# Optimization experiments

Hardware: AMD Instinct MI355X
Metric: run time of the kernel (lower is better)

The kernel has to match this reference:

```python
import jax, jax.numpy as jnp
import numpy as np

N = 50000; FIN = 64; H = 128; E = 800000; T = 8
P = 250000; D = 500000; G = 20000; V = 2000; O = 2


def _mp(h, Ws, Wn, b, edge_src, edge_dst, n):
    # mean-aggregation message passing: relu(h Ws + mean_neigh(h) Wn + b)
    deg = jax.ops.segment_sum(jnp.ones(edge_dst.shape[0], h.dtype), edge_dst, n)
    agg = jax.ops.segment_sum(h[edge_src], edge_dst, n) / jnp.maximum(deg, 1.0)[:, None]
    return jax.nn.relu(h @ Ws + agg @ Wn + b)


def _forward(x, W_enc_self, W_enc_nei, b_enc, W2_self, W2_nei, b2, Wd1, bd1, Wd2, bd2,
             counts, edge_src, edge_dst, place_idx, src_idx, t_idx, dst_nodes, dst_seg,
             group_id, variant_of_group):
    n = x.shape[0]
    p = place_idx.shape[0]
    g = variant_of_group.shape[0]
    v = counts.shape[0]
    # first encoder, then T sequential second_encoder applications (feature generations)
    h0 = _mp(x, W_enc_self, W_enc_nei, b_enc, edge_src, edge_dst, n)

    def step(h, _):
        h2 = _mp(h, W2_self, W2_nei, b2, edge_src, edge_dst, n)
        return h2, h2

    _, hs = jax.lax.scan(step, h0, None, length=T)
    feats = jnp.concatenate([h0[None], hs], axis=0)  # [T+1, N, H]

    # gather (place, src) features at the generation index of each prediction
    place_f = feats[t_idx, place_idx]                 # [P, H]
    src_f = feats[t_idx, src_idx]                     # [P, H]
    # dst feature = sum over the destination set of each prediction
    dst_f = jax.ops.segment_sum(feats[t_idx[dst_seg], dst_nodes], dst_seg, p)  # [P, H]

    cat = jnp.concatenate([place_f, src_f, dst_f], axis=-1)  # [P, 3H]
    logits = jax.nn.relu(cat @ Wd1 + bd1) @ Wd2 + bd2        # [P, O]
    logprob = jax.nn.log_softmax(logits, axis=-1)            # [P, O]

    # prev_prob: inclusive running sum of per-step logprob sums within each variant
    group_sums = jax.ops.segment_sum(logprob, group_id, g)   # [G, O]
    cum = jnp.cumsum(group_sums, axis=0)
    var_tot = jax.ops.segment_sum(group_sums, variant_of_group, v)
    var_excl = jnp.cumsum(var_tot, axis=0) - var_tot
    within = cum - var_excl[variant_of_group]                # [G, O]
    prev = within[group_id]                                  # [P, O]

    logc = jnp.log(counts / jnp.sum(counts))                 # log(count/total) per variant
    add = logprob + prev + logc[variant_of_group[group_id]][:, None]
    return jnp.zeros((n, logits.shape[-1]), x.dtype).at[place_idx].add(add)


def setup_inputs() -> dict:
    ks = jax.random.split(jax.random.key(0), 24)
    s = jnp.float32(0.05)
    f32 = jnp.float32
    i32 = jnp.int32
    return {
        "x": jax.random.normal(ks[0], (N, FIN), f32),
        "W_enc_self": jax.random.normal(ks[1], (FIN, H), f32) * s,
        "W_enc_nei": jax.random.normal(ks[2], (FIN, H), f32) * s,
        "b_enc": jax.random.normal(ks[3], (H,), f32) * s,
        "W2_self": jax.random.normal(ks[4], (H, H), f32) * s,
        "W2_nei": jax.random.normal(ks[5], (H, H), f32) * s,
        "b2": jax.random.normal(ks[6], (H,), f32) * s,
        "Wd1": jax.random.normal(ks[7], (3 * H, 3 * H), f32) * s,
        "bd1": jax.random.normal(ks[8], (3 * H,), f32) * s,
        "Wd2": jax.random.normal(ks[9], (3 * H, O), f32) * s,
        "bd2": jax.random.normal(ks[10], (O,), f32) * s,
        "counts": jax.random.uniform(ks[11], (V,), f32) + 0.5,
        "edge_src": jax.random.randint(ks[12], (E,), 0, N, i32),
        "edge_dst": jax.random.randint(ks[13], (E,), 0, N, i32),
        "place_idx": jax.random.randint(ks[14], (P,), 0, N, i32),
        "src_idx": jax.random.randint(ks[15], (P,), 0, N, i32),
        "t_idx": jax.random.randint(ks[16], (P,), 0, T + 1, i32),
        "dst_nodes": jax.random.randint(ks[17], (D,), 0, N, i32),
        "dst_seg": jnp.sort(jax.random.randint(ks[18], (D,), 0, P, i32)),
        "group_id": jnp.sort(jax.random.randint(ks[19], (P,), 0, G, i32)),
        "variant_of_group": jnp.sort(jax.random.randint(ks[20], (G,), 0, V, i32)),
    }


def reference(x, W_enc_self, W_enc_nei, b_enc, W2_self, W2_nei, b2, Wd1, bd1, Wd2, bd2,
              counts, edge_src, edge_dst, place_idx, src_idx, t_idx, dst_nodes, dst_seg,
              group_id, variant_of_group):
    return _forward(x, W_enc_self, W_enc_nei, b_enc, W2_self, W2_nei, b2, Wd1, bd1, Wd2, bd2,
                    counts, edge_src, edge_dst, place_idx, src_idx, t_idx, dst_nodes, dst_seg,
                    group_id, variant_of_group)
```

## Files before the change

kernel.cpp:

```cpp
#include <hip/hip_runtime.h>
#include <math.h>

#define NN 50000
#define FINN 64
#define HD 128
#define EE 800000
#define TT 8
#define PP 250000
#define DD 500000
#define GG 20000
#define VV 2000
#define OO 2

#define DEC_GRID 256
#define DEC_TILES ((PP + 63) / 64)

typedef short short8 __attribute__((ext_vector_type(8)));
typedef float f32x4 __attribute__((ext_vector_type(4)));

__device__ __forceinline__ unsigned short f2bf(float f) {
    unsigned int u = __float_as_uint(f);
    u += 0x7fffu + ((u >> 16) & 1u);
    return (unsigned short)(u >> 16);
}
__device__ __forceinline__ float bf2f(unsigned short u) {
    return __uint_as_float(((unsigned int)u) << 16);
}

__device__ __forceinline__ unsigned char q8(float f) {
    unsigned short u = f2bf(f);
    unsigned int e = (u >> 7) & 0xffu;
    unsigned int s = (u >> 8) & 0x80u;
    if (e < 121u) return (unsigned char)s;
    unsigned int m = u & 0x7fu;
    unsigned int m3 = m >> 4, rr = m & 0xfu;
    m3 += (rr > 8u) || (rr == 8u && (m3 & 1u));
    unsigned int ee = e - 120u;
    if (m3 == 8u) { m3 = 0u; ++ee; }
    if (ee > 15u || (ee == 15u && m3 == 7u)) { ee = 15u; m3 = 6u; }
    return (unsigned char)(s | (ee << 3) | m3);
}
__device__ __forceinline__ unsigned int dq1(unsigned int b) {
    unsigned int t = b & 0x7fu;
    unsigned int r = ((b & 0x80u) << 8) | ((t << 4) + 0x3C00u);
    return t ? r : 0u;
}

struct us8 { unsigned short v[8]; };

__device__ __forceinline__ void gload_lds16(const void* g, void* l) {
    __builtin_amdgcn_global_load_lds((__attribute__((address_space(1))) void*)g,
                                     (__attribute__((address_space(3))) void*)l, 16, 0, 0);
}

__global__ void count_k(const int* __restrict__ idx, int* __restrict__ counts, int n) {
    int i = blockIdx.x * blockDim.x + threadIdx.x;
    if (i < n) atomicAdd(&counts[idx[i]], 1);
}

__global__ void blk_sum_k(const int* __restrict__ counts, int n, int* __restrict__ bsum) {
    __shared__ int buf[256];
    int t = threadIdx.x, i = blockIdx.x * 256 + t;
    buf[t] = (i < n) ? counts[i] : 0;
    __syncthreads();
    for (int off = 128; off > 0; off >>= 1) {
        if (t < off) buf[t] += buf[t + off];
        __syncthreads();
    }
    if (t == 0) bsum[blockIdx.x] = buf[0];
}

__global__ void scan_small_k(const int* __restrict__ bsum, int nb, int* __restrict__ boff) {
    __shared__ int buf[256];
    int t = threadIdx.x;
    int v = (t < nb) ? bsum[t] : 0;
    buf[t] = v;
    __syncthreads();
    for (int off = 1; off < 256; off <<= 1) {
        int u = (t >= off) ? buf[t - off] : 0;
        __syncthreads();
        buf[t] += u;
        __syncthreads();
    }
    if (t < nb) boff[t] = buf[t] - v;
}

__global__ void rowptr_fill_k(const int* __restrict__ counts, const int* __restrict__ boff,
                              int n, int* __restrict__ rowptr, int total) {
    __shared__ int buf[256];
    int t = threadIdx.x, i = blockIdx.x * 256 + t;
    int v = (i < n) ? counts[i] : 0;
    buf[t] = v;
    __syncthreads();
    for (int off = 1; off < 256; off <<= 1) {
        int u = (t >= off) ? buf[t - off] : 0;
        __syncthreads();
        buf[t] += u;
        __syncthreads();
    }
    if (i < n) rowptr[i] = boff[blockIdx.x] + buf[t] - v;
    if (i == 0) rowptr[n] = total;
}

__global__ void lb_rowptr_k(const int* __restrict__ arr, int n, int* __restrict__ rowptr, int m) {
    int i = blockIdx.x * blockDim.x + threadIdx.x;
    if (i > m) return;
    int lo = 0, hi = n;
    while (lo < hi) {
        int mid = (lo + hi) >> 1;
        if (arr[mid] < i) lo = mid + 1; else hi = mid;
    }
    rowptr[i] = lo;
}

__global__ void fill_csr_k(const int* __restrict__ esrc, const int* __restrict__ edst,
                           const int* __restrict__ rowptr, int* __restrict__ cursor,
                           int* __restrict__ outi, int n) {
    int e = blockIdx.x * blockDim.x + threadIdx.x;
    if (e < n) {
        int d = edst[e];
        int pos = atomicAdd(&cursor[d], 1);
        outi[rowptr[d] + pos] = esrc[e];
    }
}

__global__ void hist9_k(const int* __restrict__ t_idx, int* __restrict__ hist) {
    __shared__ int l[9];
    if (threadIdx.x < 9) l[threadIdx.x] = 0;
    __syncthreads();
    int p = blockIdx.x * 256 + threadIdx.x;
    if (p < PP) atomicAdd(&l[t_idx[p]], 1);
    __syncthreads();
    if (threadIdx.x < 9) atomicAdd(&hist[threadIdx.x], l[threadIdx.x]);
}

__global__ void scan9_k(const int* __restrict__ hist, int* __restrict__ boff9) {
    if (threadIdx.x == 0) {
        int a = 0;
        for (int i = 0; i < 9; ++i) { boff9[i] = a; a += hist[i]; }
        boff9[9] = a;
    }
}

__global__ void bucket_perm_k(const int* __restrict__ t_idx, const int* __restrict__ boff9,
                              int* __restrict__ cursor9, int* __restrict__ pperm) {
    __shared__ int lcnt[9];
    __shared__ int lbase[9];
    int tid = threadIdx.x;
    int p = blockIdx.x * 256 + tid;
    if (tid < 9) lcnt[tid] = 0;
    __syncthreads();
    int t = 0, lr = 0;
    bool ok = p < PP;
    if (ok) {
        t = t_idx[p];
        lr = atomicAdd(&lcnt[t], 1);
    }
    __syncthreads();
    if (tid < 9) lbase[tid] = atomicAdd(&cursor9[tid], lcnt[tid]);
    __syncthreads();
    if (ok) pperm[boff9[t] + lbase[t] + lr] = p;
}

__global__ void prep_k(const float* __restrict__ x,
                       const float* __restrict__ Wes, const float* __restrict__ Wen,
                       const float* __restrict__ W2s, const float* __restrict__ W2n,
                       const float* __restrict__ Wd1,
                       unsigned short* __restrict__ xb, unsigned short* __restrict__ wenc_t,
                       unsigned short* __restrict__ w2_t, unsigned short* __restrict__ wd1t,
                       unsigned char* __restrict__ wd1tq) {
    int i = blockIdx.x * 256 + threadIdx.x;
    if (i < NN * FINN) xb[i] = f2bf(x[i]);
    if (i < HD * 2 * FINN) {
        int c = i / (2 * FINN), k = i - c * (2 * FINN);
        wenc_t[i] = f2bf((k < FINN) ? Wes[k * HD + c] : Wen[(k - FINN) * HD + c]);
    }
    if (i < HD * 2 * HD) {
        int c = i / (2 * HD), k = i - c * (2 * HD);
        w2_t[i] = f2bf((k < HD) ? W2s[k * HD + c] : W2n[(k - HD) * HD + c]);
    }
    if (i < 384 * 384) {
        int n = i / 384, k = i - n * 384;
        float v = Wd1[k * 384 + n];
        wd1t[i] = f2bf(v);
        wd1tq[i] = q8(v);
    }
}

template <int KIN>
__launch_bounds__(256)
__global__ void mpf_k(const unsigned short* __restrict__ hin,
                      const int* __restrict__ rowptr, const int* __restrict__ csr_src,
                      const unsigned short* __restrict__ Wt, const float* __restrict__ bias,
                      unsigned short* __restrict__ hout, unsigned char* __restrict__ houtq) {
    constexpr int CPL = KIN / 64;
    __shared__ unsigned short sm[32 * KIN];
    int tid = threadIdx.x;
    int r = tid >> 3;
    int sl = tid & 7;
    int node = blockIdx.x * 32 + r;
    int rx = r & 7;

    if (node < NN) {
        int s = rowptr[node], e = rowptr[node + 1];
        float acc[8 * CPL] = {};
        int i = s, iB = s + 1;
        int srcA = (i < e) ? csr_src[i] : 0;
        int srcB = (iB < e) ? csr_src[iB] : 0;
        while (i < e) {
            bool hB = iB < e;
            us8 vA0, vA1, vB0, vB1;
            vA0 = *(const us8*)&hin[(size_t)srcA * KIN + sl * (8 * CPL)];
            if constexpr (CPL == 2) vA1 = *(const us8*)&hin[(size_t)srcA * KIN + sl * 16 + 8];
            if (hB) {
                vB0 = *(const us8*)&hin[(size_t)srcB * KIN + sl * (8 * CPL)];
                if constexpr (CPL == 2) vB1 = *(const us8*)&hin[(size_t)srcB * KIN + sl * 16 + 8];
            }
            int iN = i + 2, iN2 = i + 3;
            srcA = (iN < e) ? csr_src[iN] : 0;
            srcB = (iN2 < e) ? csr_src[iN2] : 0;
#pragma unroll
            for (int j = 0; j < 8; ++j) acc[j] += bf2f(vA0.v[j]);
            if constexpr (CPL == 2)
#pragma unroll
                for (int j = 0; j < 8; ++j) acc[8 + j] += bf2f(vA1.v[j]);
            if (hB) {
#pragma unroll
                for (int j = 0; j < 8; ++j) acc[j] += bf2f(vB0.v[j]);
                if constexpr (CPL == 2)
#pragma unroll
                    for (int j = 0; j < 8; ++j) acc[8 + j] += bf2f(vB1.v[j]);
            }
            i = iN; iB = iN2;
        }
        float d = fmaxf((float)(e - s), 1.f);
        us8 o0, o1;
#pragma unroll
        for (int j = 0; j < 8; ++j) o0.v[j] = f2bf(acc[j] / d);
        int c0 = sl * CPL;
        *(us8*)&sm[r * KIN + ((c0 ^ rx) * 8)] = o0;
        if constexpr (CPL == 2) {
#pragma unroll
            for (int j = 0; j < 8; ++j) o1.v[j] = f2bf(acc[8 + j] / d);
            *(us8*)&sm[r * KIN + (((c0 + 1) ^ rx) * 8)] = o1;
        }
    }
    __syncthreads();

    int lane = tid & 63, w = tid >> 6;
    int cc = lane & 15, gq = lane >> 4;
    constexpr int K = 2 * KIN;
    int rloc = (w & 1) * 16 + cc;
    int rowA = blockIdx.x * 32 + rloc;
    bool rowok = rowA < NN;
    const unsigned short* hrow = hin + (size_t)rowA * KIN;
    int ch = (w >> 1) * 64;
    int rlx = rloc & 7;

    f32x4 acc2[4];
#pragma unroll
    for (int t = 0; t < 4; ++t) acc2[t] = (f32x4){0.f, 0.f, 0.f, 0.f};

#pragma unroll
    for (int k0 = 0; k0 < K; k0 += 32) {
        int k = k0 + gq * 8;
        short8 a = {0, 0, 0, 0, 0, 0, 0, 0};
        if (rowok) {
            if (k0 < KIN) a = *(const short8*)(hrow + k);
            else {
                int chunk = (k - KIN) >> 3;
                a = *(const short8*)&sm[rloc * KIN + ((chunk ^ rlx) * 8)];
            }
        }
#pragma unroll
        for (int t = 0; t < 4; ++t) {
            short8 b = *(const short8*)&Wt[(size_t)(ch + t * 16 + cc) * K + k];
            acc2[t] = __builtin_amdgcn_mfma_f32_16x16x32_bf16(a, b, acc2[t], 0, 0, 0);
        }
    }
#pragma unroll
    for (int t = 0; t < 4; ++t) {
        int col = ch + t * 16 + cc;
        float b1 = bias[col];
#pragma unroll
        for (int rj = 0; rj < 4; ++rj) {
            int grow = blockIdx.x * 32 + (w & 1) * 16 + gq * 4 + rj;
            if (grow < NN) {
                float v = fmaxf(acc2[t][rj] + b1, 0.f);
                hout[(size_t)grow * HD + col] = f2bf(v);
                houtq[(size_t)grow * HD + col] = q8(v);
            }
        }
    }
}

__launch_bounds__(256)
__global__ void dst_sum2q_k(const unsigned char* __restrict__ featsq,
                            const int* __restrict__ t_idx, const int* __restrict__ dst_nodes,
                            const int* __restrict__ dst_rowptr, const int* __restrict__ pperm,
                            unsigned char* __restrict__ dstcq) {
    int tid = threadIdx.x;
    int grp = tid >> 4;
    int fl = tid & 15;
    int pi = blockIdx.x * 16 + grp;
    if (pi >= PP) return;
    int p = pperm[pi];
    long t = t_idx[p];
    const unsigned char* base = featsq + (size_t)t * NN * HD;
    int s = dst_rowptr[p], e = dst_rowptr[p + 1];
    float acc[8] = {};
    int i = s;
    int n0 = (i < e) ? dst_nodes[i] : 0;
    int n1 = (i + 1 < e) ? dst_nodes[i + 1] : 0;
    while (i < e) {
        bool h1 = (i + 1) < e;
        unsigned long long v0 = *(const unsigned long long*)&base[(size_t)n0 * HD + fl * 8];
        unsigned long long v1 = 0;
        if (h1) v1 = *(const unsigned long long*)&base[(size_t)n1 * HD + fl * 8];
        int i2 = i + 2, i3 = i + 3;
        n0 = (i2 < e) ? dst_nodes[i2] : 0;
        n1 = (i3 < e) ? dst_nodes[i3] : 0;
#pragma unroll
        for (int j = 0; j < 8; ++j)
            acc[j] += bf2f((unsigned short)dq1((unsigned int)(v0 >> (8 * j)) & 0xffu));
        if (h1) {
#pragma unroll
            for (int j = 0; j < 8; ++j)
                acc[j] += bf2f((unsigned short)dq1((unsigned int)(v1 >> (8 * j)) & 0xffu));
        }
        i = i2;
    }
    unsigned long long ov = 0;
#pragma unroll
    for (int j = 0; j < 8; ++j) ov |= (unsigned long long)q8(acc[j]) << (8 * j);
    *(unsigned long long*)&dstcq[(size_t)pi * HD + fl * 8] = ov;
}

__global__ void
__attribute__((amdgpu_flat_work_group_size(512, 512), amdgpu_waves_per_eu(2, 2)))
dec10_k(const unsigned char* __restrict__ featsq,
        const unsigned char* __restrict__ dstcq,
        const int* __restrict__ place_idx, const int* __restrict__ src_idx,
        const int* __restrict__ t_idx, const int* __restrict__ group_id,
        const int* __restrict__ pperm,
        const unsigned char* __restrict__ wd1tq,
        const float* __restrict__ bd1, const float* __restrict__ Wd2,
        const float* __restrict__ bd2, float* __restrict__ logprob,
        float* __restrict__ group_sums) {
    __shared__ unsigned char buf[3][192 * 128];
    __shared__ unsigned int rb[3][192];
    __shared__ float lpart[3][8][64][2];

    int tid = threadIdx.x;
    int lane = tid & 63, w = tid >> 6;
    int cc = lane & 15, gq = lane >> 4;
    int bid = blockIdx.x;

    int row = min(tid, 191);
    int sec = row >> 6, pl = row & 63;
    const int* nptr = (sec == 0) ? place_idx : src_idx;
    unsigned int dstc_off = (unsigned int)(dstcq - featsq);

    int nt = (DEC_TILES - 1 - bid) / DEC_GRID + 1;
    float b20 = bd2[0], b21 = bd2[1];

    if (tid < 192) {
#pragma unroll
        for (int s3 = 0; s3 < 3; ++s3) {
            int pic = min((bid + s3 * DEC_GRID) * 64 + pl, PP - 1);
            int p = pperm[pic];
            rb[s3][tid] = (sec == 2) ? (dstc_off + (unsigned int)pic * 128u)
                                     : (unsigned int)(((unsigned)t_idx[p] * NN + (unsigned)nptr[p]) * 128u);
        }
    }
    int p3 = pperm[min((bid + 3 * DEC_GRID) * 64 + pl, PP - 1)];
    int tOld = t_idx[p3], nOld = nptr[p3];
    int pCur = pperm[min((bid + 4 * DEC_GRID) * 64 + pl, PP - 1)];
    int opPP = 0, opP = 0, ogP = 0;

    unsigned long long breg[36];
    float b1r[3], w0r[3], w1r[3];
    {
        const unsigned char* bbase = wd1tq + ((long)(w * 48 + cc) * 384 + gq * 8);
#pragma unroll
        for (int kk = 0; kk < 12; ++kk)
#pragma unroll
            for (int t = 0; t < 3; ++t)
                breg[kk * 3 + t] = *(const unsigned long long*)(bbase + (long)t * 16 * 384 + kk * 32);
#pragma unroll
        for (int t = 0; t < 3; ++t) {
            int col = w * 48 + t * 16 + cc;
            b1r[t] = bd1[col];
            w0r[t] = Wd2[col * 2 + 0];
            w1r[t] = Wd2[col * 2 + 1];
        }
    }
    __syncthreads();

    int rsub8 = lane >> 3, chunk8 = lane & 7;

#define STAGE(slot_)                                                                 \
    {                                                                                \
        _Pragma("unroll")                                                            \
        for (int i = 0; i < 3; ++i) {                                                \
            int r = w * 24 + i * 8 + rsub8;                                          \
            const unsigned char* src = featsq + rb[slot_][r] +                       \
                                       ((unsigned)(chunk8 ^ (r & 7)) << 4);          \
            gload_lds16(src, &buf[slot_][(w * 24 + i * 8) * 128]);                   \
        }                                                                            \
    }

#define OUTPUT(tile_, slot_, opv_, ogv_)                                             \
    {                                                                                \
        int pi = (bid + (tile_) * DEC_GRID) * 64 + w * 16 + cc;                      \
        if (pi < PP) {                                                               \
            float l0 = b20, l1 = b21;                                                \
            _Pragma("unroll")                                                        \
            for (int w2 = 0; w2 < 8; ++w2) {                                         \
                l0 += lpart[slot_][w2][w * 16 + cc][0];                              \
                l1 += lpart[slot_][w2][w * 16 + cc][1];                              \
            }                                                                        \
            float mm = fmaxf(l0, l1);                                                \
            float lse = mm + logf(expf(l0 - mm) + expf(l1 - mm));                    \
            float lp0 = l0 - lse, lp1 = l1 - lse;                                    \
            logprob[(opv_)*2 + 0] = lp0;                                             \
            logprob[(opv_)*2 + 1] = lp1;                                             \
            atomicAdd(&group_sums[(ogv_)*2 + 0], lp0);                               \
            atomicAdd(&group_sums[(ogv_)*2 + 1], lp1);                               \
        }                                                                            \
    }

    STAGE(0);
    STAGE(1);

    for (int k = 0; k < nt; ++k) {
        int slot = k % 3;

        int opN = pperm[min((bid + k * DEC_GRID) * 64 + (w & 3) * 16 + cc, PP - 1)];
        int ogN = group_id[opP];
        int pNew = pperm[min((bid + (k + 5) * DEC_GRID) * 64 + pl, PP - 1)];
        int tNew = t_idx[pCur];
        int nNew = nptr[pCur];
        __builtin_amdgcn_sched_barrier(0);

        if (k + 2 < nt) STAGE((k + 2) % 3);
        __builtin_amdgcn_sched_barrier(0);

        if (k + 2 < nt) {
            if (k >= 2) { asm volatile("s_waitcnt vmcnt(16)" ::: "memory"); }
            else        { asm volatile("s_waitcnt vmcnt(11)" ::: "memory"); }
        } else if (k + 1 < nt) {
            asm volatile("s_waitcnt vmcnt(13)" ::: "memory");
        } else {
            asm volatile("s_waitcnt vmcnt(5)" ::: "memory");
        }
        __builtin_amdgcn_s_barrier();
        __builtin_amdgcn_sched_barrier(0);

        if (k >= 2 && w < 4 && lane < 16) OUTPUT(k - 2, (k - 2) % 3, opPP, ogP);

        {
            const unsigned char* bufc = &buf[slot][0];
            f32x4 acc[4][3];
#pragma unroll
            for (int s = 0; s < 4; ++s)
#pragma unroll
                for (int t = 0; t < 3; ++t) acc[s][t] = (f32x4){0.f, 0.f, 0.f, 0.f};

#pragma unroll
            for (int kk = 0; kk < 12; ++kk) {
                int seck = kk >> 2;
                int eb = (kk & 3) * 32 + gq * 8;
                int c16 = eb >> 4, sub = (eb >> 3) & 1;
                long a_c[4];
#pragma unroll
                for (int s = 0; s < 4; ++s) {
                    int lrow = seck * 64 + s * 16 + cc;
                    a_c[s] = *(const long*)
                        &bufc[lrow * 128 + ((c16 ^ (lrow & 7)) << 4) + sub * 8];
                }
#pragma unroll
                for (int t = 0; t < 3; ++t)
#pragma unroll
                    for (int s = 0; s < 4; ++s)
                        acc[s][t] = __builtin_amdgcn_mfma_f32_16x16x32_fp8_fp8(
                            a_c[s], (long)breg[kk * 3 + t], acc[s][t], 0, 0, 0);
            }

#pragma unroll
            for (int s = 0; s < 4; ++s) {
                float p0[4], p1[4];
#pragma unroll
                for (int r = 0; r < 4; ++r) { p0[r] = 0.f; p1[r] = 0.f; }
#pragma unroll
                for (int t = 0; t < 3; ++t) {
#pragma unroll
                    for (int r = 0; r < 4; ++r) {
                        float h = fmaxf(acc[s][t][r] + b1r[t], 0.f);
                        p0[r] += h * w0r[t];
                        p1[r] += h * w1r[t];
                    }
                }
#pragma unroll
                for (int m = 1; m < 16; m <<= 1)
#pragma unroll
                    for (int r = 0; r < 4; ++r) {
                        p0[r] += __shfl_xor(p0[r], m);
                        p1[r] += __shfl_xor(p1[r], m);
                    }
                if (cc == 0) {
#pragma unroll
                    for (int r = 0; r < 4; ++r) {
                        int orow = s * 16 + gq * 4 + r;
                        lpart[slot][w][orow][0] = p0[r];
                        lpart[slot][w][orow][1] = p1[r];
                    }
                }
            }
        }

        if (tid < 192) {
            int picw = min((bid + (k + 3) * DEC_GRID) * 64 + pl, PP - 1);
            rb[(k + 3) % 3][tid] = (sec == 2)
                ? (dstc_off + (unsigned int)picw * 128u)
                : (unsigned int)(((unsigned)tOld * NN + (unsigned)nOld) * 128u);
        }
        tOld = tNew; nOld = nNew; pCur = pNew;
        opPP = opP; opP = opN; ogP = ogN;

        asm volatile("s_waitcnt lgkmcnt(0)" ::: "memory");
        __builtin_amdgcn_s_barrier();
        __builtin_amdgcn_sched_barrier(0);
    }

    if (w < 4 && lane < 16) {
        OUTPUT(nt - 2, (nt - 2) % 3, opPP, ogP);
        int ogLast = group_id[opP];
        OUTPUT(nt - 1, (nt - 1) % 3, opP, ogLast);
    }
#undef STAGE
#undef OUTPUT
}

__global__ void within_total_k(const float* __restrict__ group_sums,
                               const int* __restrict__ var_rowptr,
                               const float* __restrict__ counts,
                               float* __restrict__ within, float* __restrict__ total) {
    __shared__ float buf[256];
    int tid = threadIdx.x;
    float s = 0.f;
    for (int i = tid; i < VV; i += 256) s += counts[i];
    buf[tid] = s;
    __syncthreads();
    for (int off = 128; off > 0; off >>= 1) {
        if (tid < off) buf[tid] += buf[tid + off];
        __syncthreads();
    }
    if (tid == 0) total[0] = buf[0];
    for (int v = tid; v < VV; v += 256) {
        int gs = var_rowptr[v], ge = var_rowptr[v + 1];
        float r0 = 0.f, r1 = 0.f;
        for (int g = gs; g < ge; ++g) {
            r0 += group_sums[2 * g + 0];
            r1 += group_sums[2 * g + 1];
            within[2 * g + 0] = r0;
            within[2 * g + 1] = r1;
        }
    }
}

__global__ void final_k(const float* __restrict__ logprob, const float* __restrict__ within,
                        const int* __restrict__ group_id, const int* __restrict__ vog,
                        const float* __restrict__ counts, const float* __restrict__ total,
                        const int* __restrict__ place_idx, float* __restrict__ outp) {
    int p = blockIdx.x * blockDim.x + threadIdx.x;
    if (p >= PP) return;
    int g = group_id[p];
    int v = vog[g];
    float lc = logf(counts[v]) - logf(total[0]);
    int node = place_idx[p];
    atomicAdd(&outp[node * 2 + 0], logprob[p * 2 + 0] + within[g * 2 + 0] + lc);
    atomicAdd(&outp[node * 2 + 1], logprob[p * 2 + 1] + within[g * 2 + 1] + lc);
}

extern "C" void kernel_launch(void* const* d_in, const int* in_sizes, int n_in,
                              void* d_out, int out_size, void* d_ws, size_t ws_size,
                              hipStream_t stream) {
    const float* x          = (const float*)d_in[0];
    const float* W_enc_self = (const float*)d_in[1];
    const float* W_enc_nei  = (const float*)d_in[2];
    const float* b_enc      = (const float*)d_in[3];
    const float* W2_self    = (const float*)d_in[4];
    const float* W2_nei     = (const float*)d_in[5];
    const float* b2         = (const float*)d_in[6];
    const float* Wd1        = (const float*)d_in[7];
    const float* bd1        = (const float*)d_in[8];
    const float* Wd2        = (const float*)d_in[9];
    const float* bd2        = (const float*)d_in[10];
    const float* counts     = (const float*)d_in[11];
    const int* edge_src     = (const int*)d_in[12];
    const int* edge_dst     = (const int*)d_in[13];
    const int* place_idx    = (const int*)d_in[14];
    const int* src_idx      = (const int*)d_in[15];
    const int* t_idx        = (const int*)d_in[16];
    const int* dst_nodes    = (const int*)d_in[17];
    const int* dst_seg      = (const int*)d_in[18];
    const int* group_id     = (const int*)d_in[19];
    const int* variant_of_group = (const int*)d_in[20];
    float* outp = (float*)d_out;

    const int NB = (NN + 255) / 256;

    unsigned short* rot0 = (unsigned short*)d_ws;
    unsigned short* rot1 = rot0 + (size_t)NN * HD;
    unsigned short* xb   = rot1 + (size_t)NN * HD;
    unsigned char* featsq = (unsigned char*)(xb + (size_t)NN * FINN);
    unsigned char* dstcq  = featsq + (size_t)(TT + 1) * NN * HD;
    unsigned short* wenc_t = (unsigned short*)(dstcq + (size_t)PP * HD);
    unsigned short* w2_t   = wenc_t + HD * 2 * FINN;
    unsigned short* wd1t   = w2_t + HD * 2 * HD;
    unsigned char* wd1tq   = (unsigned char*)(wd1t + 384 * 384);
    int* zr = (int*)(wd1tq + 384 * 384);
    int* csr_counts   = zr;
    int* csr_cursor   = csr_counts + NN;
    float* group_sums = (float*)(csr_cursor + NN);
    int* hist9        = (int*)(group_sums + 2 * GG);
    int* cursor9      = hist9 + 9;
    size_t zero_words = (size_t)NN + NN + 2 * GG + 18;
    int* bsum       = cursor9 + 9;
    int* boff       = bsum + 256;
    int* boff9      = boff + 256;
    int* csr_rowptr = boff9 + 16;
    int* dst_rowptr = csr_rowptr + (NN + 1);
    int* var_rowptr = dst_rowptr + (PP + 1);
    int* csr_src    = var_rowptr + (VV + 1);
    int* pperm      = csr_src + EE;
    float* logprob  = (float*)(pperm + PP);
    float* within   = logprob + 2 * PP;
    float* total_counts = within + 2 * GG;

    hipMemsetAsync(zr, 0, zero_words * 4, stream);
    hipMemsetAsync(d_out, 0, (size_t)out_size * sizeof(float), stream);

    prep_k<<<(NN * FINN + 255) / 256, 256, 0, stream>>>(x, W_enc_self, W_enc_nei, W2_self,
                                                        W2_nei, Wd1, xb, wenc_t, w2_t,
                                                        wd1t, wd1tq);
    count_k<<<(EE + 255) / 256, 256, 0, stream>>>(edge_dst, csr_counts, EE);
    blk_sum_k<<<NB, 256, 0, stream>>>(csr_counts, NN, bsum);
    scan_small_k<<<1, 256, 0, stream>>>(bsum, NB, boff);
    rowptr_fill_k<<<NB, 256, 0, stream>>>(csr_counts, boff, NN, csr_rowptr, EE);
    fill_csr_k<<<(EE + 255) / 256, 256, 0, stream>>>(edge_src, edge_dst, csr_rowptr,
                                                     csr_cursor, csr_src, EE);
    lb_rowptr_k<<<(PP + 256) / 256, 256, 0, stream>>>(dst_seg, DD, dst_rowptr, PP);
    lb_rowptr_k<<<(VV + 256) / 256, 256, 0, stream>>>(variant_of_group, GG, var_rowptr, VV);
    hist9_k<<<(PP + 255) / 256, 256, 0, stream>>>(t_idx, hist9);
    scan9_k<<<1, 64, 0, stream>>>(hist9, boff9);
    bucket_perm_k<<<(PP + 255) / 256, 256, 0, stream>>>(t_idx, boff9, cursor9, pperm);

    const int NB32 = (NN + 31) / 32;
    for (int r = 0; r <= TT; ++r) {
        const unsigned short* hin = (r == 0) ? xb : ((r & 1) ? rot0 : rot1);
        unsigned short* hout = (r & 1) ? rot1 : rot0;
        unsigned char* houtq = featsq + (size_t)r * NN * HD;
        if (r == 0)
            mpf_k<FINN><<<NB32, 256, 0, stream>>>(hin, csr_rowptr, csr_src, wenc_t, b_enc,
                                                  hout, houtq);
        else
            mpf_k<HD><<<NB32, 256, 0, stream>>>(hin, csr_rowptr, csr_src, w2_t, b2,
                                                hout, houtq);
    }

    dst_sum2q_k<<<(PP + 15) / 16, 256, 0, stream>>>(featsq, t_idx, dst_nodes, dst_rowptr,
                                                    pperm, dstcq);
    dec10_k<<<DEC_GRID, 512, 0, stream>>>(featsq, dstcq, place_idx, src_idx, t_idx,
                                          group_id, pperm, wd1tq, bd1, Wd2, bd2,
                                          logprob, group_sums);

    within_total_k<<<1, 256, 0, stream>>>(group_sums, var_rowptr, counts, within, total_counts);
    final_k<<<(PP + 255) / 256, 256, 0, stream>>>(logprob, within, group_id, variant_of_group,
                                                  counts, total_counts, place_idx, outp);
}
```

Before: 954.9 us.

## Gather FP8 neighbor features in message passing and deepen decoder pipeline

The message-passing neighbor aggregation now reads the 8-bit quantized copy of each layer's features instead of bf16, which halves gather traffic. The input x gets its own quantized copy for the same purpose. Dequantization goes through a hardware packed fp8-to-f32 conversion builtin when one is available, and the dst-sum kernel uses it too. The decoder's LDS staging grows from a 3-slot to a 4-slot ring with retuned waitcnt values, to hide more load latency. In exchange, aggregation accuracy drops to fp8 precision and the kernel uses more LDS, which may lower occupancy.

```diff
diff --git a/kernel.cpp b/kernel.cpp
--- a/kernel.cpp
+++ b/kernel.cpp
@@ -17,6 +17,8 @@
 
 typedef short short8 __attribute__((ext_vector_type(8)));
 typedef float f32x4 __attribute__((ext_vector_type(4)));
+typedef unsigned int uint2v __attribute__((ext_vector_type(2)));
+typedef unsigned int uint4v __attribute__((ext_vector_type(4)));
 
 __device__ __forceinline__ unsigned short f2bf(float f) {
     unsigned int u = __float_as_uint(f);
@@ -46,6 +48,22 @@
     return t ? r : 0u;
 }
 
+#if __has_builtin(__builtin_amdgcn_cvt_pk_f32_fp8)
+typedef float float2v __attribute__((ext_vector_type(2)));
+__device__ __forceinline__ void acc_u32(float* acc, unsigned int w) {
+    float2v lo = __builtin_amdgcn_cvt_pk_f32_fp8(w, false);
+    float2v hi = __builtin_amdgcn_cvt_pk_f32_fp8(w, true);
+    acc[0] += lo[0]; acc[1] += lo[1]; acc[2] += hi[0]; acc[3] += hi[1];
+}
+#else
+__device__ __forceinline__ void acc_u32(float* acc, unsigned int w) {
+    acc[0] += bf2f((unsigned short)dq1(w & 0xffu));
+    acc[1] += bf2f((unsigned short)dq1((w >> 8) & 0xffu));
+    acc[2] += bf2f((unsigned short)dq1((w >> 16) & 0xffu));
+    acc[3] += bf2f((unsigned short)dq1((w >> 24) & 0xffu));
+}
+#endif
+
 struct us8 { unsigned short v[8]; };
 
 __device__ __forceinline__ void gload_lds16(const void* g, void* l) {
@@ -166,11 +184,16 @@
                        const float* __restrict__ Wes, const float* __restrict__ Wen,
                        const float* __restrict__ W2s, const float* __restrict__ W2n,
                        const float* __restrict__ Wd1,
-                       unsigned short* __restrict__ xb, unsigned short* __restrict__ wenc_t,
+                       unsigned short* __restrict__ xb, unsigned char* __restrict__ xbq,
+                       unsigned short* __restrict__ wenc_t,
                        unsigned short* __restrict__ w2_t, unsigned short* __restrict__ wd1t,
                        unsigned char* __restrict__ wd1tq) {
     int i = blockIdx.x * 256 + threadIdx.x;
-    if (i < NN * FINN) xb[i] = f2bf(x[i]);
+    if (i < NN * FINN) {
+        float v = x[i];
+        xb[i] = f2bf(v);
+        xbq[i] = q8(v);
+    }
     if (i < HD * 2 * FINN) {
         int c = i / (2 * FINN), k = i - c * (2 * FINN);
         wenc_t[i] = f2bf((k < FINN) ? Wes[k * HD + c] : Wen[(k - FINN) * HD + c]);
@@ -189,10 +212,11 @@
 
 template <int KIN>
 __launch_bounds__(256)
-__global__ void mpf_k(const unsigned short* __restrict__ hin,
-                      const int* __restrict__ rowptr, const int* __restrict__ csr_src,
-                      const unsigned short* __restrict__ Wt, const float* __restrict__ bias,
-                      unsigned short* __restrict__ hout, unsigned char* __restrict__ houtq) {
+__global__ void mpf2_k(const unsigned short* __restrict__ hin,
+                       const unsigned char* __restrict__ hinq,
+                       const int* __restrict__ rowptr, const int* __restrict__ csr_src,
+                       const unsigned short* __restrict__ Wt, const float* __restrict__ bias,
+                       unsigned short* __restrict__ hout, unsigned char* __restrict__ houtq) {
     constexpr int CPL = KIN / 64;
     __shared__ unsigned short sm[32 * KIN];
     int tid = threadIdx.x;
@@ -209,27 +233,28 @@
         int srcB = (iB < e) ? csr_src[iB] : 0;
         while (i < e) {
             bool hB = iB < e;
-            us8 vA0, vA1, vB0, vB1;
-            vA0 = *(const us8*)&hin[(size_t)srcA * KIN + sl * (8 * CPL)];
-            if constexpr (CPL == 2) vA1 = *(const us8*)&hin[(size_t)srcA * KIN + sl * 16 + 8];
-            if (hB) {
-                vB0 = *(const us8*)&hin[(size_t)srcB * KIN + sl * (8 * CPL)];
-                if constexpr (CPL == 2) vB1 = *(const us8*)&hin[(size_t)srcB * KIN + sl * 16 + 8];
+            uint4v vA, vB;
+            uint2v wA, wB;
+            if constexpr (CPL == 2) {
+                vA = *(const uint4v*)&hinq[(size_t)srcA * KIN + sl * 16];
+                if (hB) vB = *(const uint4v*)&hinq[(size_t)srcB * KIN + sl * 16];
+            } else {
+                wA = *(const uint2v*)&hinq[(size_t)srcA * KIN + sl * 8];
+                if (hB) wB = *(const uint2v*)&hinq[(size_t)srcB * KIN + sl * 8];
             }
             int iN = i + 2, iN2 = i + 3;
             srcA = (iN < e) ? csr_src[iN] : 0;
             srcB = (iN2 < e) ? csr_src[iN2] : 0;
-#pragma unroll
-            for (int j = 0; j < 8; ++j) acc[j] += bf2f(vA0.v[j]);
-            if constexpr (CPL == 2)
-#pragma unroll
-                for (int j = 0; j < 8; ++j) acc[8 + j] += bf2f(vA1.v[j]);
-            if (hB) {
-#pragma unroll
-                for (int j = 0; j < 8; ++j) acc[j] += bf2f(vB0.v[j]);
-                if constexpr (CPL == 2)
-#pragma unroll
-                    for (int j = 0; j < 8; ++j) acc[8 + j] += bf2f(vB1.v[j]);
+            if constexpr (CPL == 2) {
+                acc_u32(acc + 0, vA[0]); acc_u32(acc + 4, vA[1]);
+                acc_u32(acc + 8, vA[2]); acc_u32(acc + 12, vA[3]);
+                if (hB) {
+                    acc_u32(acc + 0, vB[0]); acc_u32(acc + 4, vB[1]);
+                    acc_u32(acc + 8, vB[2]); acc_u32(acc + 12, vB[3]);
+                }
+            } else {
+                acc_u32(acc + 0, wA[0]); acc_u32(acc + 4, wA[1]);
+                if (hB) { acc_u32(acc + 0, wB[0]); acc_u32(acc + 4, wB[1]); }
             }
             i = iN; iB = iN2;
         }
@@ -314,20 +339,14 @@
     int n1 = (i + 1 < e) ? dst_nodes[i + 1] : 0;
     while (i < e) {
         bool h1 = (i + 1) < e;
-        unsigned long long v0 = *(const unsigned long long*)&base[(size_t)n0 * HD + fl * 8];
-        unsigned long long v1 = 0;
-        if (h1) v1 = *(const unsigned long long*)&base[(size_t)n1 * HD + fl * 8];
+        uint2v v0 = *(const uint2v*)&base[(size_t)n0 * HD + fl * 8];
+        uint2v v1;
+        if (h1) v1 = *(const uint2v*)&base[(size_t)n1 * HD + fl * 8];
         int i2 = i + 2, i3 = i + 3;
         n0 = (i2 < e) ? dst_nodes[i2] : 0;
         n1 = (i3 < e) ? dst_nodes[i3] : 0;
-#pragma unroll
-        for (int j = 0; j < 8; ++j)
-            acc[j] += bf2f((unsigned short)dq1((unsigned int)(v0 >> (8 * j)) & 0xffu));
-        if (h1) {
-#pragma unroll
-            for (int j = 0; j < 8; ++j)
-                acc[j] += bf2f((unsigned short)dq1((unsigned int)(v1 >> (8 * j)) & 0xffu));
-        }
+        acc_u32(acc + 0, v0[0]); acc_u32(acc + 4, v0[1]);
+        if (h1) { acc_u32(acc + 0, v1[0]); acc_u32(acc + 4, v1[1]); }
         i = i2;
     }
     unsigned long long ov = 0;
@@ -338,7 +357,7 @@
 
 __global__ void
 __attribute__((amdgpu_flat_work_group_size(512, 512), amdgpu_waves_per_eu(2, 2)))
-dec10_k(const unsigned char* __restrict__ featsq,
+dec11_k(const unsigned char* __restrict__ featsq,
         const unsigned char* __restrict__ dstcq,
         const int* __restrict__ place_idx, const int* __restrict__ src_idx,
         const int* __restrict__ t_idx, const int* __restrict__ group_id,
@@ -347,8 +366,8 @@
         const float* __restrict__ bd1, const float* __restrict__ Wd2,
         const float* __restrict__ bd2, float* __restrict__ logprob,
         float* __restrict__ group_sums) {
-    __shared__ unsigned char buf[3][192 * 128];
-    __shared__ unsigned int rb[3][192];
+    __shared__ unsigned char buf[4][192 * 128];
+    __shared__ unsigned int rb[4][192];
     __shared__ float lpart[3][8][64][2];
 
     int tid = threadIdx.x;
@@ -366,16 +385,16 @@
 
     if (tid < 192) {
 #pragma unroll
-        for (int s3 = 0; s3 < 3; ++s3) {
-            int pic = min((bid + s3 * DEC_GRID) * 64 + pl, PP - 1);
+        for (int s4 = 0; s4 < 4; ++s4) {
+            int pic = min((bid + s4 * DEC_GRID) * 64 + pl, PP - 1);
             int p = pperm[pic];
-            rb[s3][tid] = (sec == 2) ? (dstc_off + (unsigned int)pic * 128u)
+            rb[s4][tid] = (sec == 2) ? (dstc_off + (unsigned int)pic * 128u)
                                      : (unsigned int)(((unsigned)t_idx[p] * NN + (unsigned)nptr[p]) * 128u);
         }
     }
-    int p3 = pperm[min((bid + 3 * DEC_GRID) * 64 + pl, PP - 1)];
-    int tOld = t_idx[p3], nOld = nptr[p3];
-    int pCur = pperm[min((bid + 4 * DEC_GRID) * 64 + pl, PP - 1)];
+    int p4 = pperm[min((bid + 4 * DEC_GRID) * 64 + pl, PP - 1)];
+    int tOld = t_idx[p4], nOld = nptr[p4];
+    int pCur = pperm[min((bid + 5 * DEC_GRID) * 64 + pl, PP - 1)];
     int opPP = 0, opP = 0, ogP = 0;
 
     unsigned long long breg[36];
@@ -432,27 +451,31 @@
 
     STAGE(0);
     STAGE(1);
+    STAGE(2);
 
     for (int k = 0; k < nt; ++k) {
-        int slot = k % 3;
+        int slot = k & 3;
 
         int opN = pperm[min((bid + k * DEC_GRID) * 64 + (w & 3) * 16 + cc, PP - 1)];
         int ogN = group_id[opP];
-        int pNew = pperm[min((bid + (k + 5) * DEC_GRID) * 64 + pl, PP - 1)];
+        int pNew = pperm[min((bid + (k + 6) * DEC_GRID) * 64 + pl, PP - 1)];
         int tNew = t_idx[pCur];
         int nNew = nptr[pCur];
         __builtin_amdgcn_sched_barrier(0);
 
-        if (k + 2 < nt) STAGE((k + 2) % 3);
+        if (k + 3 < nt) STAGE((k + 3) & 3);
         __builtin_amdgcn_sched_barrier(0);
 
-        if (k + 2 < nt) {
-            if (k >= 2) { asm volatile("s_waitcnt vmcnt(16)" ::: "memory"); }
-            else        { asm volatile("s_waitcnt vmcnt(11)" ::: "memory"); }
+        if (k + 3 < nt) {
+            if (k >= 2)      { asm volatile("s_waitcnt vmcnt(24)" ::: "memory"); }
+            else if (k == 1) { asm volatile("s_waitcnt vmcnt(19)" ::: "memory"); }
+            else             { asm volatile("s_waitcnt vmcnt(14)" ::: "memory"); }
+        } else if (k + 2 < nt) {
+            asm volatile("s_waitcnt vmcnt(21)" ::: "memory");
         } else if (k + 1 < nt) {
-            asm volatile("s_waitcnt vmcnt(13)" ::: "memory");
+            asm volatile("s_waitcnt vmcnt(18)" ::: "memory");
         } else {
-            asm volatile("s_waitcnt vmcnt(5)" ::: "memory");
+            asm volatile("s_waitcnt vmcnt(15)" ::: "memory");
         }
         __builtin_amdgcn_s_barrier();
         __builtin_amdgcn_sched_barrier(0);
@@ -512,16 +535,16 @@
 #pragma unroll
                     for (int r = 0; r < 4; ++r) {
                         int orow = s * 16 + gq * 4 + r;
-                        lpart[slot][w][orow][0] = p0[r];
-                        lpart[slot][w][orow][1] = p1[r];
+                        lpart[k % 3][w][orow][0] = p0[r];
+                        lpart[k % 3][w][orow][1] = p1[r];
                     }
                 }
             }
         }
 
         if (tid < 192) {
-            int picw = min((bid + (k + 3) * DEC_GRID) * 64 + pl, PP - 1);
-            rb[(k + 3) % 3][tid] = (sec == 2)
+            int picw = min((bid + (k + 4) * DEC_GRID) * 64 + pl, PP - 1);
+            rb[k & 3][tid] = (sec == 2)
                 ? (dstc_off + (unsigned int)picw * 128u)
                 : (unsigned int)(((unsigned)tOld * NN + (unsigned)nOld) * 128u);
         }
@@ -614,7 +637,8 @@
     unsigned short* rot0 = (unsigned short*)d_ws;
     unsigned short* rot1 = rot0 + (size_t)NN * HD;
     unsigned short* xb   = rot1 + (size_t)NN * HD;
-    unsigned char* featsq = (unsigned char*)(xb + (size_t)NN * FINN);
+    unsigned char* xbq   = (unsigned char*)(xb + (size_t)NN * FINN);
+    unsigned char* featsq = xbq + (size_t)NN * FINN;
     unsigned char* dstcq  = featsq + (size_t)(TT + 1) * NN * HD;
     unsigned short* wenc_t = (unsigned short*)(dstcq + (size_t)PP * HD);
     unsigned short* w2_t   = wenc_t + HD * 2 * FINN;
@@ -643,7 +667,7 @@
     hipMemsetAsync(d_out, 0, (size_t)out_size * sizeof(float), stream);
 
     prep_k<<<(NN * FINN + 255) / 256, 256, 0, stream>>>(x, W_enc_self, W_enc_nei, W2_self,
-                                                        W2_nei, Wd1, xb, wenc_t, w2_t,
+                                                        W2_nei, Wd1, xb, xbq, wenc_t, w2_t,
                                                         wd1t, wd1tq);
     count_k<<<(EE + 255) / 256, 256, 0, stream>>>(edge_dst, csr_counts, EE);
     blk_sum_k<<<NB, 256, 0, stream>>>(csr_counts, NN, bsum);
@@ -660,19 +684,20 @@
     const int NB32 = (NN + 31) / 32;
     for (int r = 0; r <= TT; ++r) {
         const unsigned short* hin = (r == 0) ? xb : ((r & 1) ? rot0 : rot1);
+        const unsigned char* hinq = (r == 0) ? xbq : featsq + (size_t)(r - 1) * NN * HD;
         unsigned short* hout = (r & 1) ? rot1 : rot0;
         unsigned char* houtq = featsq + (size_t)r * NN * HD;
         if (r == 0)
-            mpf_k<FINN><<<NB32, 256, 0, stream>>>(hin, csr_rowptr, csr_src, wenc_t, b_enc,
-                                                  hout, houtq);
+            mpf2_k<FINN><<<NB32, 256, 0, stream>>>(hin, hinq, csr_rowptr, csr_src, wenc_t,
+                                                   b_enc, hout, houtq);
         else
-            mpf_k<HD><<<NB32, 256, 0, stream>>>(hin, csr_rowptr, csr_src, w2_t, b2,
-                                                hout, houtq);
+            mpf2_k<HD><<<NB32, 256, 0, stream>>>(hin, hinq, csr_rowptr, csr_src, w2_t,
+                                                 b2, hout, houtq);
     }
 
     dst_sum2q_k<<<(PP + 15) / 16, 256, 0, stream>>>(featsq, t_idx, dst_nodes, dst_rowptr,
                                                     pperm, dstcq);
-    dec10_k<<<DEC_GRID, 512, 0, stream>>>(featsq, dstcq, place_idx, src_idx, t_idx,
+    dec11_k<<<DEC_GRID, 512, 0, stream>>>(featsq, dstcq, place_idx, src_idx, t_idx,
                                           group_id, pperm, wd1tq, bd1, Wd2, bd2,
                                           logprob, group_sums);
 
```

New measurement: 910.2 us. -4.7%, faster.
